# Performance work log

Hardware: AMD Instinct MI355X
Metric: run time of the kernel (lower is better)

Reference implementation:

```python
import jax, jax.numpy as jnp
import numpy as np

TEMPERATURE = 0.2

def setup_inputs() -> dict:
    key = jax.random.key(0)
    k1, k2 = jax.random.split(key)
    B, D = 4096, 128
    emb_i = jax.random.normal(k1, (B, D), dtype=jnp.float32)
    emb_j = jax.random.normal(k2, (B, D), dtype=jnp.float32)
    return {"emb_i": emb_i, "emb_j": emb_j}

def reference(emb_i, emb_j):
    # L2-normalize each embedding row, concat -> z: [2B, D]
    z_i = emb_i / jnp.linalg.norm(emb_i, axis=1, keepdims=True)
    z_j = emb_j / jnp.linalg.norm(emb_j, axis=1, keepdims=True)
    z = jnp.concatenate([z_i, z_j], axis=0)          # [2B, D]
    N2 = z.shape[0]
    N = N2 // 2
    # cosine similarity of normalized vectors == dot product
    sim = z @ z.T                                    # [2B, 2B]
    logits = sim / TEMPERATURE
    # denominator excludes only the diagonal (k != i)
    diag_mask = jnp.eye(N2, dtype=bool)
    masked = jnp.where(diag_mask, -jnp.inf, logits)
    lse = jax.nn.logsumexp(masked, axis=1)           # [2B]
    # positive pair for row i is i+N (mod 2N)
    pos_idx = jnp.concatenate([jnp.arange(N) + N, jnp.arange(N)])
    pos_logits = jnp.take_along_axis(logits, pos_idx[:, None], axis=1)[:, 0]
    # loss = (1/2N) * sum_i -log( exp(pos_i) / sum_{k!=i} exp(logits[i,k]) )
    loss = jnp.mean(lse - pos_logits)
    return loss
```

## Files before the change

### kernel.cpp

```cpp
#include <hip/hip_runtime.h>
#include <hip/hip_bf16.h>
#include <hip/hip_fp8.h>

typedef __attribute__((ext_vector_type(4))) float f32x4;
typedef long long i64;

#define EXP_SCALE 7.213475204444817f

__device__ __forceinline__ float fast_exp2(float x) {
#if __has_builtin(__builtin_amdgcn_exp2f)
  return __builtin_amdgcn_exp2f(x);
#else
  return exp2f(x);
#endif
}


__global__ __launch_bounds__(256) void k_normalize(
    const float* __restrict__ emb_i, const float* __restrict__ emb_j,
    unsigned char* __restrict__ z, float* __restrict__ rowsum,
    float* __restrict__ out)
{
  if (blockIdx.x == 0 && threadIdx.x == 0) out[0] = 0.0f;
  if (threadIdx.x < 16) rowsum[(blockIdx.x << 4) + threadIdx.x] = 0.0f;
  const int t = threadIdx.x;
  const int c = t >> 4;
  const int sub = t & 15;
  const int row = (blockIdx.x << 4) + c;
  const float* src = (row < 4096) ? (emb_i + row * 128) : (emb_j + (row - 4096) * 128);
  float4 v0 = reinterpret_cast<const float4*>(src)[sub * 2];
  float4 v1 = reinterpret_cast<const float4*>(src)[sub * 2 + 1];
  float ss = v0.x*v0.x + v0.y*v0.y + v0.z*v0.z + v0.w*v0.w
           + v1.x*v1.x + v1.y*v1.y + v1.z*v1.z + v1.w*v1.w;
  #pragma unroll
  for (int m = 1; m < 16; m <<= 1) ss += __shfl_xor(ss, m, 64);
  float rinv = 1.0f / sqrtf(ss);
  unsigned char st[8];
  st[0] = __hip_fp8_e4m3(v0.x * rinv).__x;
  st[1] = __hip_fp8_e4m3(v0.y * rinv).__x;
  st[2] = __hip_fp8_e4m3(v0.z * rinv).__x;
  st[3] = __hip_fp8_e4m3(v0.w * rinv).__x;
  st[4] = __hip_fp8_e4m3(v1.x * rinv).__x;
  st[5] = __hip_fp8_e4m3(v1.y * rinv).__x;
  st[6] = __hip_fp8_e4m3(v1.z * rinv).__x;
  st[7] = __hip_fp8_e4m3(v1.w * rinv).__x;
  unsigned char* dst = z + blockIdx.x * 2048 + (sub >> 2) * 512 +
                       (((sub & 3) << 4) + c) * 8;
  *reinterpret_cast<i64*>(dst) = *reinterpret_cast<i64*>(st);
}

__global__ __launch_bounds__(256, 4) void k_simlse(
    const unsigned char* __restrict__ z,
    float* __restrict__ rowsum,
    float* __restrict__ rowpos)
{
  const int w = threadIdx.x >> 6;
  const int lane = threadIdx.x & 63;
  const int q = lane >> 4;
  const int c = lane & 15;

  int ch = 0;
  while ((int)blockIdx.x >= 4 * (ch + 1) * (ch + 2)) ++ch;
  const int rb = blockIdx.x - 4 * ch * (ch + 1);
  const int R0 = rb << 6;
  const bool upper = (rb < (ch << 3));

  i64 a[4][4];
  {
    const unsigned char* ap = z + (R0 >> 4) * 2048 + (lane << 3);
    #pragma unroll
    for (int rg = 0; rg < 4; ++rg)
      #pragma unroll
      for (int kk = 0; kk < 4; ++kk)
        a[rg][kk] = *reinterpret_cast<const i64*>(ap + rg * 2048 + kk * 512);
  }

  float acc[4][4];
  #pragma unroll
  for (int rg = 0; rg < 4; ++rg)
    #pragma unroll
    for (int e = 0; e < 4; ++e) acc[rg][e] = 0.0f;
  float pacc[4] = {0.f, 0.f, 0.f, 0.f};
  float colp[8];
  #pragma unroll
  for (int i = 0; i < 8; ++i) colp[i] = 0.0f;

  __shared__ float lsum[4][64];
  __shared__ float lpos[4][16];

  const int ct0 = (ch << 5) + w;
  const unsigned char* bwave = z + ct0 * 2048 + (lane << 3);

  const int pos0t = ((R0 + 4096) & 8191) >> 4;
  const int ipb = ((pos0t >> 5) == ch) ? ((pos0t & 31) >> 2) : -99;

  i64 b0[4], b1[4];
  auto ldb = [&](i64 (&dst)[4], int idx) {
    const unsigned char* p = bwave + idx * 8192;
    dst[0] = *reinterpret_cast<const i64*>(p);
    dst[1] = *reinterpret_cast<const i64*>(p + 512);
    dst[2] = *reinterpret_cast<const i64*>(p + 1024);
    dst[3] = *reinterpret_cast<const i64*>(p + 1536);
  };

  auto process = [&](const i64 (&bb)[4], int i) {
    f32x4 cc[4];
    #pragma unroll
    for (int rr = 0; rr < 4; ++rr) cc[rr] = f32x4{0.f, 0.f, 0.f, 0.f};
    #pragma unroll
    for (int kk = 0; kk < 4; ++kk)
      #pragma unroll
      for (int rr = 0; rr < 4; ++rr)
        cc[rr] = __builtin_amdgcn_mfma_f32_16x16x32_fp8_fp8(
            a[rr][kk], bb[kk], cc[rr], 0, 0, 0);
    float cp0 = 0.0f, cp1 = 0.0f;
    #pragma unroll
    for (int rr = 0; rr < 4; ++rr)
      #pragma unroll
      for (int e = 0; e < 4; ++e) {
        float tv = fast_exp2(__builtin_fmaf(cc[rr][e], EXP_SCALE, -EXP_SCALE));
        acc[rr][e] += tv;
        if (upper) { if (rr & 1) cp1 += tv; else cp0 += tv; }
      }
    if (upper) colp[i] = cp0 + cp1;
    if (i == ipb) {
      #pragma unroll
      for (int rr = 0; rr < 4; ++rr) {
        if (rr == w) {
          #pragma unroll
          for (int e = 0; e < 4; ++e)
            if (c == ((q << 2) + e)) pacc[e] = cc[rr][e] * 5.0f;
        }
      }
    }
  };

  ldb(b0, 0);
  #pragma unroll 1
  for (int i = 0; i < 8; i += 2) {
    ldb(b1, i + 1);
    process(b0, i);
    if (i + 2 < 8) ldb(b0, i + 2);
    process(b1, i + 1);
  }

  if (upper) {
    #pragma unroll
    for (int i = 0; i < 8; ++i) {
      float v = colp[i];
      v += __shfl_xor(v, 16, 64);
      v += __shfl_xor(v, 32, 64);
      if (lane < 16)
        atomicAdd(&rowsum[((ct0 + (i << 2)) << 4) + c], v);
    }
  }

  #pragma unroll
  for (int m = 1; m < 16; m <<= 1) {
    #pragma unroll
    for (int rg = 0; rg < 4; ++rg)
      #pragma unroll
      for (int e = 0; e < 4; ++e)
        acc[rg][e] += __shfl_xor(acc[rg][e], m, 64);
    #pragma unroll
    for (int e = 0; e < 4; ++e) pacc[e] += __shfl_xor(pacc[e], m, 64);
  }

  if (c == 0) {
    #pragma unroll
    for (int rg = 0; rg < 4; ++rg)
      #pragma unroll
      for (int e = 0; e < 4; ++e)
        lsum[w][rg * 16 + (q << 2) + e] = acc[rg][e];
    #pragma unroll
    for (int e = 0; e < 4; ++e) lpos[w][(q << 2) + e] = pacc[e];
  }
  __syncthreads();

  if (threadIdx.x < 64) {
    const int t = threadIdx.x;
    float s = lsum[0][t] + lsum[1][t] + lsum[2][t] + lsum[3][t];
    atomicAdd(&rowsum[R0 + t], s);
    if (ipb != -99)
      rowpos[R0 + t] = lpos[t >> 4][t & 15];
  }
}

__global__ __launch_bounds__(256) void k_finish(
    const float* __restrict__ rowsum, const float* __restrict__ rowpos,
    float* __restrict__ out)
{
  const int r = blockIdx.x * 256 + threadIdx.x;
  float tot = rowsum[r] - 1.0f;
  float v = 5.0f + logf(tot) - rowpos[r & 4095];
  #pragma unroll
  for (int m = 1; m < 64; m <<= 1) v += __shfl_xor(v, m, 64);
  __shared__ float red[4];
  if ((threadIdx.x & 63) == 0) red[threadIdx.x >> 6] = v;
  __syncthreads();
  if (threadIdx.x == 0)
    atomicAdd(out, (red[0] + red[1] + red[2] + red[3]) * (1.0f / 8192.0f));
}

extern "C" void kernel_launch(void* const* d_in, const int* in_sizes, int n_in,
                              void* d_out, int out_size, void* d_ws, size_t ws_size,
                              hipStream_t stream) {
  const float* emb_i = (const float*)d_in[0];
  const float* emb_j = (const float*)d_in[1];
  unsigned char* z = (unsigned char*)d_ws;
  float* rowsum = (float*)((char*)d_ws + (1 << 20));
  float* rowpos = rowsum + 8192;
  float* out = (float*)d_out;

  k_normalize<<<512, 256, 0, stream>>>(emb_i, emb_j, z, rowsum, out);
  k_simlse<<<1088, 256, 0, stream>>>(z, rowsum, rowpos);
  k_finish<<<32, 256, 0, stream>>>(rowsum, rowpos, out);
}
```

Measured before the change: 76.79 us.

## Fuse normalize, similarity-LSE and finish into one persistent kernel with atomic counters

Merges the three kernels into a single launch. The first 512 blocks normalize tiles and bump a global counter, all blocks spin until normalization completes, and the last block to finish does the final reduction. A memset zeroes the accumulators and counters. This removes two kernel launch gaps in exchange for a spin-wait grid barrier, with a fallback that recomputes the needed tiles locally if waiting takes too long. It relies on enough blocks being co-resident and adds a memset call.

```diff
diff --git a/kernel.cpp b/kernel.cpp
--- a/kernel.cpp
+++ b/kernel.cpp
@@ -16,17 +16,14 @@
 }
 
 
-__global__ __launch_bounds__(256) void k_normalize(
-    const float* __restrict__ emb_i, const float* __restrict__ emb_j,
-    unsigned char* __restrict__ z, float* __restrict__ rowsum,
-    float* __restrict__ out)
+__device__ __forceinline__ void norm_tile(
+    int tile, const float* __restrict__ emb_i, const float* __restrict__ emb_j,
+    unsigned char* __restrict__ z)
 {
-  if (blockIdx.x == 0 && threadIdx.x == 0) out[0] = 0.0f;
-  if (threadIdx.x < 16) rowsum[(blockIdx.x << 4) + threadIdx.x] = 0.0f;
   const int t = threadIdx.x;
   const int c = t >> 4;
   const int sub = t & 15;
-  const int row = (blockIdx.x << 4) + c;
+  const int row = (tile << 4) + c;
   const float* src = (row < 4096) ? (emb_i + row * 128) : (emb_j + (row - 4096) * 128);
   float4 v0 = reinterpret_cast<const float4*>(src)[sub * 2];
   float4 v1 = reinterpret_cast<const float4*>(src)[sub * 2 + 1];
@@ -44,25 +41,22 @@
   st[5] = __hip_fp8_e4m3(v1.y * rinv).__x;
   st[6] = __hip_fp8_e4m3(v1.z * rinv).__x;
   st[7] = __hip_fp8_e4m3(v1.w * rinv).__x;
-  unsigned char* dst = z + blockIdx.x * 2048 + (sub >> 2) * 512 +
+  unsigned char* dst = z + tile * 2048 + (sub >> 2) * 512 +
                        (((sub & 3) << 4) + c) * 8;
-  *reinterpret_cast<i64*>(dst) = *reinterpret_cast<i64*>(st);
-}
-
-__global__ __launch_bounds__(256, 4) void k_simlse(
-    const unsigned char* __restrict__ z,
-    float* __restrict__ rowsum,
-    float* __restrict__ rowpos)
+  i64 val;
+  __builtin_memcpy(&val, st, 8);
+  __hip_atomic_store(reinterpret_cast<i64*>(dst), val,
+                     __ATOMIC_RELAXED, __HIP_MEMORY_SCOPE_AGENT);
+}
+
+__device__ __forceinline__ void do_cell_body(
+    int ch, int rb, int R0, const unsigned char* __restrict__ z,
+    float* __restrict__ rowsum, float* __restrict__ rowpos)
 {
   const int w = threadIdx.x >> 6;
   const int lane = threadIdx.x & 63;
   const int q = lane >> 4;
   const int c = lane & 15;
-
-  int ch = 0;
-  while ((int)blockIdx.x >= 4 * (ch + 1) * (ch + 2)) ++ch;
-  const int rb = blockIdx.x - 4 * ch * (ch + 1);
-  const int R0 = rb << 6;
   const bool upper = (rb < (ch << 3));
 
   i64 a[4][4];
@@ -182,24 +176,81 @@
     float s = lsum[0][t] + lsum[1][t] + lsum[2][t] + lsum[3][t];
     atomicAdd(&rowsum[R0 + t], s);
     if (ipb != -99)
-      rowpos[R0 + t] = lpos[t >> 4][t & 15];
-  }
-}
-
-__global__ __launch_bounds__(256) void k_finish(
-    const float* __restrict__ rowsum, const float* __restrict__ rowpos,
+      __hip_atomic_store(&rowpos[R0 + t], lpos[t >> 4][t & 15],
+                         __ATOMIC_RELAXED, __HIP_MEMORY_SCOPE_AGENT);
+  }
+}
+
+__global__ __launch_bounds__(256, 4) void k_all(
+    const float* __restrict__ emb_i, const float* __restrict__ emb_j,
+    unsigned char* __restrict__ z, float* __restrict__ rowsum,
+    int* __restrict__ ctrs, float* __restrict__ rowpos,
     float* __restrict__ out)
 {
-  const int r = blockIdx.x * 256 + threadIdx.x;
-  float tot = rowsum[r] - 1.0f;
-  float v = 5.0f + logf(tot) - rowpos[r & 4095];
-  #pragma unroll
-  for (int m = 1; m < 64; m <<= 1) v += __shfl_xor(v, m, 64);
-  __shared__ float red[4];
-  if ((threadIdx.x & 63) == 0) red[threadIdx.x >> 6] = v;
-  __syncthreads();
-  if (threadIdx.x == 0)
-    atomicAdd(out, (red[0] + red[1] + red[2] + red[3]) * (1.0f / 8192.0f));
+  const int bid = blockIdx.x;
+
+  if (bid < 512) {
+    norm_tile(bid, emb_i, emb_j, z);
+    asm volatile("s_waitcnt vmcnt(0)" ::: "memory");
+    if (threadIdx.x == 0)
+      __hip_atomic_fetch_add(&ctrs[0], 1, __ATOMIC_RELAXED,
+                             __HIP_MEMORY_SCOPE_AGENT);
+  }
+
+  int ch = 0;
+  while (bid >= 4 * (ch + 1) * (ch + 2)) ++ch;
+  const int rb = bid - 4 * ch * (ch + 1);
+  const int R0 = rb << 6;
+
+  __shared__ int sflag;
+  if (threadIdx.x == 0) {
+    int it = 0, fb = 0;
+    while (__hip_atomic_load(&ctrs[0], __ATOMIC_RELAXED,
+                             __HIP_MEMORY_SCOPE_AGENT) < 512) {
+      __builtin_amdgcn_s_sleep(8);
+      if (++it > (1 << 17)) { fb = 1; break; }
+    }
+    sflag = fb;
+  }
+  __syncthreads();
+  if (sflag) {
+    #pragma unroll 1
+    for (int k = 0; k < 4; ++k) norm_tile((R0 >> 4) + k, emb_i, emb_j, z);
+    #pragma unroll 1
+    for (int k = 0; k < 32; ++k) norm_tile((ch << 5) + k, emb_i, emb_j, z);
+    asm volatile("s_waitcnt vmcnt(0)" ::: "memory");
+    __syncthreads();
+  }
+
+  do_cell_body(ch, rb, R0, z, rowsum, rowpos);
+
+  __syncthreads();
+  __shared__ int sfin;
+  if (threadIdx.x == 0) {
+    int old = __hip_atomic_fetch_add(&ctrs[32], 1, __ATOMIC_RELAXED,
+                                     __HIP_MEMORY_SCOPE_AGENT);
+    sfin = (old == 1087);
+  }
+  __syncthreads();
+
+  if (sfin) {
+    float part = 0.0f;
+    #pragma unroll 1
+    for (int r = threadIdx.x; r < 8192; r += 256) {
+      float tot = __hip_atomic_load(&rowsum[r], __ATOMIC_RELAXED,
+                                    __HIP_MEMORY_SCOPE_AGENT) - 1.0f;
+      float p = __hip_atomic_load(&rowpos[r & 4095], __ATOMIC_RELAXED,
+                                  __HIP_MEMORY_SCOPE_AGENT);
+      part += 5.0f + logf(tot) - p;
+    }
+    #pragma unroll
+    for (int m = 1; m < 64; m <<= 1) part += __shfl_xor(part, m, 64);
+    __shared__ float red[4];
+    if ((threadIdx.x & 63) == 0) red[threadIdx.x >> 6] = part;
+    __syncthreads();
+    if (threadIdx.x == 0)
+      out[0] = (red[0] + red[1] + red[2] + red[3]) * (1.0f / 8192.0f);
+  }
 }
 
 extern "C" void kernel_launch(void* const* d_in, const int* in_sizes, int n_in,
@@ -209,10 +260,10 @@
   const float* emb_j = (const float*)d_in[1];
   unsigned char* z = (unsigned char*)d_ws;
   float* rowsum = (float*)((char*)d_ws + (1 << 20));
-  float* rowpos = rowsum + 8192;
+  int* ctrs = (int*)((char*)d_ws + (1 << 20) + 32768);
+  float* rowpos = (float*)((char*)d_ws + (1 << 20) + 33024);
   float* out = (float*)d_out;
 
-  k_normalize<<<512, 256, 0, stream>>>(emb_i, emb_j, z, rowsum, out);
-  k_simlse<<<1088, 256, 0, stream>>>(z, rowsum, rowpos);
-  k_finish<<<32, 256, 0, stream>>>(rowsum, rowpos, out);
-}
+  hipMemsetAsync((char*)d_ws + (1 << 20), 0, 33024, stream);
+  k_all<<<1088, 256, 0, stream>>>(emb_i, emb_j, z, rowsum, ctrs, rowpos, out);
+}
```

After: 116.3 us. 51.4% more time.

## Replace atomic row/column sum accumulation with per-block partial buffers reduced in finish kernel

Applied to the files above, without the earlier changes.

Instead of atomically adding row and column exp-sums into a shared rowsum array, each block of the triangular similarity kernel writes its row partials and column partials to dedicated slots, and the finish kernel sums them per row. This removes atomic contention and the need to zero rowsum in the normalize kernel. The block-to-chunk mapping loop is also replaced with a sqrt-based closed form. In exchange, the finish kernel reads roughly 2.5 MB of partials with only 32 blocks, which may become a serial bottleneck.

```diff
diff --git a/kernel.cpp b/kernel.cpp
--- a/kernel.cpp
+++ b/kernel.cpp
@@ -18,11 +18,9 @@
 
 __global__ __launch_bounds__(256) void k_normalize(
     const float* __restrict__ emb_i, const float* __restrict__ emb_j,
-    unsigned char* __restrict__ z, float* __restrict__ rowsum,
-    float* __restrict__ out)
+    unsigned char* __restrict__ z, float* __restrict__ out)
 {
   if (blockIdx.x == 0 && threadIdx.x == 0) out[0] = 0.0f;
-  if (threadIdx.x < 16) rowsum[(blockIdx.x << 4) + threadIdx.x] = 0.0f;
   const int t = threadIdx.x;
   const int c = t >> 4;
   const int sub = t & 15;
@@ -51,17 +49,20 @@
 
 __global__ __launch_bounds__(256, 4) void k_simlse(
     const unsigned char* __restrict__ z,
-    float* __restrict__ rowsum,
+    float* __restrict__ rpart,
+    float* __restrict__ cpart,
     float* __restrict__ rowpos)
 {
   const int w = threadIdx.x >> 6;
   const int lane = threadIdx.x & 63;
   const int q = lane >> 4;
   const int c = lane & 15;
-
-  int ch = 0;
-  while ((int)blockIdx.x >= 4 * (ch + 1) * (ch + 2)) ++ch;
-  const int rb = blockIdx.x - 4 * ch * (ch + 1);
+  const int bid = blockIdx.x;
+
+  int ch = (int)((sqrtf((float)(bid + 1)) - 1.0f) * 0.5f);
+  if (bid >= 4 * (ch + 1) * (ch + 2)) ++ch;
+  else if (bid < 4 * ch * (ch + 1)) --ch;
+  const int rb = bid - 4 * ch * (ch + 1);
   const int R0 = rb << 6;
   const bool upper = (rb < (ch << 3));
 
@@ -145,13 +146,14 @@
   }
 
   if (upper) {
+    const int cbase = 2048 * ch * (ch - 1) + (rb << 9);
     #pragma unroll
     for (int i = 0; i < 8; ++i) {
       float v = colp[i];
       v += __shfl_xor(v, 16, 64);
       v += __shfl_xor(v, 32, 64);
       if (lane < 16)
-        atomicAdd(&rowsum[((ct0 + (i << 2)) << 4) + c], v);
+        cpart[cbase + ((w + (i << 2)) << 4) + c] = v;
     }
   }
 
@@ -180,18 +182,35 @@
   if (threadIdx.x < 64) {
     const int t = threadIdx.x;
     float s = lsum[0][t] + lsum[1][t] + lsum[2][t] + lsum[3][t];
-    atomicAdd(&rowsum[R0 + t], s);
+    rpart[(ch << 13) + R0 + t] = s;
     if (ipb != -99)
       rowpos[R0 + t] = lpos[t >> 4][t & 15];
   }
 }
 
 __global__ __launch_bounds__(256) void k_finish(
-    const float* __restrict__ rowsum, const float* __restrict__ rowpos,
-    float* __restrict__ out)
+    const float* __restrict__ rpart, const float* __restrict__ cpart,
+    const float* __restrict__ rowpos, float* __restrict__ out)
 {
   const int r = blockIdx.x * 256 + threadIdx.x;
-  float tot = rowsum[r] - 1.0f;
+  const int chr = r >> 9;
+
+  float rs = 0.0f;
+  #pragma unroll 4
+  for (int ch = chr; ch < 16; ++ch) rs += rpart[(ch << 13) + r];
+
+  const int nrb = chr << 3;
+  const float* cb = cpart + 2048 * chr * (chr - 1) + (r & 511);
+  float cs0 = 0.f, cs1 = 0.f, cs2 = 0.f, cs3 = 0.f;
+  #pragma unroll 2
+  for (int rb = 0; rb < nrb; rb += 4) {
+    cs0 += cb[(rb + 0) << 9];
+    cs1 += cb[(rb + 1) << 9];
+    cs2 += cb[(rb + 2) << 9];
+    cs3 += cb[(rb + 3) << 9];
+  }
+
+  float tot = rs + ((cs0 + cs1) + (cs2 + cs3)) - 1.0f;
   float v = 5.0f + logf(tot) - rowpos[r & 4095];
   #pragma unroll
   for (int m = 1; m < 64; m <<= 1) v += __shfl_xor(v, m, 64);
@@ -208,11 +227,12 @@
   const float* emb_i = (const float*)d_in[0];
   const float* emb_j = (const float*)d_in[1];
   unsigned char* z = (unsigned char*)d_ws;
-  float* rowsum = (float*)((char*)d_ws + (1 << 20));
-  float* rowpos = rowsum + 8192;
+  float* rpart = (float*)((char*)d_ws + (1 << 20));
+  float* cpart = (float*)((char*)d_ws + (1 << 20) + (512 << 10));
+  float* rowpos = (float*)((char*)d_ws + (1 << 20) + (512 << 10) + 1966080);
   float* out = (float*)d_out;
 
-  k_normalize<<<512, 256, 0, stream>>>(emb_i, emb_j, z, rowsum, out);
-  k_simlse<<<1088, 256, 0, stream>>>(z, rowsum, rowpos);
-  k_finish<<<32, 256, 0, stream>>>(rowsum, rowpos, out);
-}
+  k_normalize<<<512, 256, 0, stream>>>(emb_i, emb_j, z, out);
+  k_simlse<<<1088, 256, 0, stream>>>(z, rpart, cpart, rowpos);
+  k_finish<<<32, 256, 0, stream>>>(rpart, cpart, rowpos, out);
+}
```

After: 80.01 us. +4.2%, slower.
